# Kernel tuning notes

Measured on AMD Instinct MI355X. Metric: run time of the kernel, lower is better.

Reference implementation:

```python
import jax, jax.numpy as jnp
import numpy as np

NUM_HEADS = 16
ROPE_BASE = 10000.0

def rotate_half(x):
    h = x.shape[-1] // 2
    return jnp.concatenate([-x[..., h:], x[..., :h]], axis=-1)

def rope_cos_sin(seq_len, head_dim, dtype):
    inv_freq = 1.0 / (ROPE_BASE ** (jnp.arange(0, head_dim, 2, dtype=jnp.float32) / head_dim))
    t = jnp.arange(seq_len, dtype=jnp.float32)
    freqs = jnp.outer(t, inv_freq)              # [N, hd/2]
    emb = jnp.concatenate([freqs, freqs], -1)   # [N, hd]
    return jnp.cos(emb).astype(dtype), jnp.sin(emb).astype(dtype)

def setup_inputs() -> dict:
    key = jax.random.key(0)
    ks = jax.random.split(key, 5)
    B, N, D = 2, 2048, 1024
    s = 1.0 / np.sqrt(D)
    return {
        "x": jax.random.normal(ks[0], (B, N, D), jnp.float32),
        "attention_mask": jnp.ones((B, N), jnp.int32),
        "Wq": jax.random.normal(ks[1], (D, D), jnp.float32) * s,
        "Wk": jax.random.normal(ks[2], (D, D), jnp.float32) * s,
        "Wv": jax.random.normal(ks[3], (D, D), jnp.float32) * s,
        "Wo": jax.random.normal(ks[4], (D, D), jnp.float32) * s,
    }

def reference(x, attention_mask, Wq, Wk, Wv, Wo):
    B, N, D = x.shape
    H = NUM_HEADS
    hd = D // H
    scale = hd ** -0.5
    # projections (nn.Linear: x @ W.T), split heads -> [B, H, N, hd]
    q = jnp.einsum('bnd,ed->bne', x, Wq).reshape(B, N, H, hd).transpose(0, 2, 1, 3)
    k = jnp.einsum('bnd,ed->bne', x, Wk).reshape(B, N, H, hd).transpose(0, 2, 1, 3)
    v = jnp.einsum('bnd,ed->bne', x, Wv).reshape(B, N, H, hd).transpose(0, 2, 1, 3)
    cos, sin = rope_cos_sin(N, hd, x.dtype)     # [N, hd]
    cos = cos[None, None]; sin = sin[None, None]
    q = q * cos + rotate_half(q) * sin
    k = k * cos + rotate_half(k) * sin
    attn = jnp.einsum('bhqd,bhkd->bhqk', q, k) * scale
    mask = attention_mask.astype(bool)[:, None, None, :]        # [B,1,1,N]
    attn = jnp.where(mask, attn, -jnp.inf)
    all_masked = (attention_mask.sum(-1) == 0)[:, None, None, None]
    attn = jnp.where(all_masked, 0.0, attn)
    attn = jax.nn.softmax(attn, axis=-1)
    out = jnp.einsum('bhqk,bhkd->bhqd', attn, v)
    out = out.transpose(0, 2, 1, 3).reshape(B, N, D)
    return jnp.einsum('bnd,ed->bne', out, Wo)
```

## Files before the change

kernel.cpp:

```cpp
#include <hip/hip_runtime.h>
#include <math.h>

#define BATCH 2
#define SEQ   2048
#define DM    1024
#define NH    16
#define HD    64
#define MTOT  (BATCH*SEQ)

typedef short v8s __attribute__((ext_vector_type(8)));
typedef short v4s __attribute__((ext_vector_type(4)));
typedef float v4f __attribute__((ext_vector_type(4)));

#define MFMA16(a, b, c) __builtin_amdgcn_mfma_f32_16x16x32_bf16((a), (b), (c), 0, 0, 0)

__device__ __forceinline__ short f2b(float f) {
    union { float f; unsigned u; } v; v.f = f;
    return (short)((v.u + 0x8000u) >> 16);
}

__device__ __forceinline__ float fexp2(float x) {
    float r; asm("v_exp_f32 %0, %1" : "=v"(r) : "v"(x)); return r;
}

__device__ __forceinline__ void gload16(const void* g, void* lds) {
    __builtin_amdgcn_global_load_lds(
        (const __attribute__((address_space(1))) void*)g,
        (__attribute__((address_space(3))) void*)lds, 16, 0, 0);
}

__device__ __forceinline__ void rope_cs(int n, float f_rev, float* c, float* s) {
    float rev = (float)n * f_rev;
    float t = rev - floorf(rev);
    float ang = t * 6.283185307179586f;
    *c = __cosf(ang);
    *s = __sinf(ang);
}

#define L2_1E4_D32 0.4152410118609203f
#define INV2PI     0.15915494309189535f
#define QSCALE     0.18033688011112042f

__global__ __launch_bounds__(256) void cvt_all_kernel(
    const float* __restrict__ x,  const float* __restrict__ wq,
    const float* __restrict__ wk, const float* __restrict__ wv,
    const float* __restrict__ wo, short* __restrict__ dst)
{
    int i = blockIdx.x * 256 + threadIdx.x;
    const float* src; int off;
    if (i < (1 << 19)) { src = x; off = i; }
    else {
        int j = i - (1 << 19);
        int wsel = j >> 17;
        off = j & ((1 << 17) - 1);
        src = (wsel == 0) ? wq : (wsel == 1) ? wk : (wsel == 2) ? wv : wo;
    }
    const float4* s4 = (const float4*)src;
    float4 a = s4[2 * off], b = s4[2 * off + 1];
    v8s p;
    p[0] = f2b(a.x); p[1] = f2b(a.y); p[2] = f2b(a.z); p[3] = f2b(a.w);
    p[4] = f2b(b.x); p[5] = f2b(b.y); p[6] = f2b(b.z); p[7] = f2b(b.w);
    *(v8s*)&dst[8 * i] = p;
}

__global__ __launch_bounds__(256, 3) void qkv_rope_mfma(
    const short* __restrict__ xb, const short* __restrict__ Wqb,
    const short* __restrict__ Wkb, const short* __restrict__ Wvb,
    short* __restrict__ K, short* __restrict__ Vt, short* __restrict__ Qb)
{
    const int zz = blockIdx.z;
    const short* __restrict__ Wb = (zz == 0) ? Wkb : (zz == 1) ? Wvb : Wqb;
    const int m0 = blockIdx.x * 128, e00 = blockIdx.y * 128;
    const int tid = threadIdx.x;
    const int w = tid >> 6, lane = tid & 63, lq = lane >> 4, lr = lane & 15;
    const int wm = w >> 1, wn = w & 1;

    __shared__ union {
        struct { short As[128][32]; short Bs[128][32]; } p1;
        short Css[128][136];
    } u;

    v4f acc[4][4];
    #pragma unroll
    for (int i = 0; i < 4; ++i)
        for (int j = 0; j < 4; ++j)
            for (int r = 0; r < 4; ++r) acc[i][j][r] = 0.f;

    const int gr = lane >> 2, gc = 8 * (lane & 3);
    for (int k0 = 0; k0 < DM; k0 += 32) {
        __syncthreads();
        gload16(&xb[(size_t)(m0 + 32 * w      + gr) * DM + k0 + gc], &u.p1.As[32 * w][0]);
        gload16(&xb[(size_t)(m0 + 32 * w + 16 + gr) * DM + k0 + gc], &u.p1.As[32 * w + 16][0]);
        gload16(&Wb[(size_t)(e00 + 32 * w      + gr) * DM + k0 + gc], &u.p1.Bs[32 * w][0]);
        gload16(&Wb[(size_t)(e00 + 32 * w + 16 + gr) * DM + k0 + gc], &u.p1.Bs[32 * w + 16][0]);
        __syncthreads();
        v8s af[4], bf[4];
        #pragma unroll
        for (int i = 0; i < 4; ++i)
            af[i] = *(const v8s*)&u.p1.As[64 * wm + 16 * i + lr][8 * lq];
        #pragma unroll
        for (int j = 0; j < 4; ++j)
            bf[j] = *(const v8s*)&u.p1.Bs[64 * wn + 16 * j + lr][8 * lq];
        #pragma unroll
        for (int i = 0; i < 4; ++i)
            #pragma unroll
            for (int j = 0; j < 4; ++j)
                acc[i][j] = MFMA16(af[i], bf[j], acc[i][j]);
    }
    __syncthreads();

    const int b = m0 >> 11, n00 = m0 & (SEQ - 1);

    if (zz != 1) {
        short* __restrict__ dst = (zz == 0) ? K : Qb;
        const float sc = (zz == 0) ? 1.0f : QSCALE;
        float f0 = exp2f(-(float)lr * L2_1E4_D32) * INV2PI;
        float f1 = exp2f(-(float)(16 + lr) * L2_1E4_D32) * INV2PI;
        #pragma unroll
        for (int i = 0; i < 4; ++i) {
            #pragma unroll
            for (int r = 0; r < 4; ++r) {
                int row = 64 * wm + 16 * i + 4 * lq + r;
                int n = n00 + row;
                float c0v, s0v, c1v, s1v;
                rope_cs(n, f0, &c0v, &s0v);
                rope_cs(n, f1, &c1v, &s1v);
                float q0 = acc[i][0][r], q1 = acc[i][1][r];
                float q2 = acc[i][2][r], q3 = acc[i][3][r];
                u.Css[row][64 * wn + lr]      = f2b(sc * (q0 * c0v - q2 * s0v));
                u.Css[row][64 * wn + 16 + lr] = f2b(sc * (q1 * c1v - q3 * s1v));
                u.Css[row][64 * wn + 32 + lr] = f2b(sc * (q2 * c0v + q0 * s0v));
                u.Css[row][64 * wn + 48 + lr] = f2b(sc * (q3 * c1v + q1 * s1v));
            }
        }
        __syncthreads();
        int row = tid >> 1, hh = tid & 1;
        int h = (e00 >> 6) + hh;
        int n = n00 + row;
        size_t base = (((size_t)(b * NH + h)) * SEQ + n) * HD;
        #pragma unroll
        for (int p = 0; p < 8; ++p)
            *(v8s*)&dst[base + 8 * p] = *(const v8s*)&u.Css[row][64 * hh + 8 * p];
    } else {
        #pragma unroll
        for (int i = 0; i < 4; ++i) {
            #pragma unroll
            for (int j = 0; j < 4; ++j) {
                v4s t;
                #pragma unroll
                for (int r = 0; r < 4; ++r) t[r] = f2b(acc[i][j][r]);
                *(v4s*)&u.Css[64 * wn + 16 * j + lr][64 * wm + 16 * i + 4 * lq] = t;
            }
        }
        __syncthreads();
        int c = tid >> 1, half = (tid & 1) * 64;
        int h = (e00 + c) >> 6, d = (e00 + c) & 63;
        size_t base = (((size_t)(b * NH + h)) * HD + d) * SEQ + n00 + half;
        #pragma unroll
        for (int p = 0; p < 8; ++p)
            *(v8s*)&Vt[base + 8 * p] = *(const v8s*)&u.Css[c][half + 8 * p];
    }
}

#define SWZ(tile, row, bo) ((char*)&(tile)[row][0] + ((bo) ^ (((row) & 7) << 4)))

__global__ __launch_bounds__(512, 4) void attn_mfma(
    const short* __restrict__ Qb, const short* __restrict__ K,
    const short* __restrict__ Vt, const int* __restrict__ mask,
    short* __restrict__ O)
{
    const int m0 = blockIdx.x * 128, h = blockIdx.y;
    const int b = m0 >> 11, n0 = m0 & (SEQ - 1), bh = b * NH + h;
    const int tid = threadIdx.x;
    const int w = tid >> 6, lane = tid & 63, lq = lane >> 4, lr = lane & 15;

    __shared__ short Ks[128][64];
    __shared__ short Vs[64][128];
    __shared__ short Ps[128][64];
    __shared__ float mbias[128];

    const short* __restrict__ Qh = Qb + (size_t)bh * SEQ * HD;
    v8s aq[2];
    #pragma unroll
    for (int ks = 0; ks < 2; ++ks)
        aq[ks] = *(const v8s*)&Qh[(size_t)(n0 + 16 * w + lr) * HD + 32 * ks + 8 * lq];

    float lacc[4] = {0.f, 0.f, 0.f, 0.f};
    v4f o[4];
    #pragma unroll
    for (int nt = 0; nt < 4; ++nt)
        for (int r = 0; r < 4; ++r) o[nt][r] = 0.f;

    const int kr = tid >> 2, kc = (tid & 3) * 16;
    const int kb = 32 * (tid & 3);
    const int krh = kr & 63;
    const int pkr = 64 * (kr >> 6) + 16 * (krh & 3) + (krh >> 2);
    const int vr = tid >> 3, vc = (tid & 7) * 16;
    const int vb = 32 * (tid & 7);
    const short* __restrict__ Kb = K + (size_t)bh * SEQ * HD;
    const short* __restrict__ Vb = Vt + (size_t)bh * HD * SEQ;

    v8s k1 = *(const v8s*)&Kb[(size_t)kr * HD + kc];
    v8s k2 = *(const v8s*)&Kb[(size_t)kr * HD + kc + 8];
    v8s v1 = *(const v8s*)&Vb[(size_t)vr * SEQ + vc];
    v8s v2 = *(const v8s*)&Vb[(size_t)vr * SEQ + vc + 8];
    int mnext = ((tid & 3) == 0) ? mask[b * SEQ + kr] : 0;

    for (int c0 = 0; c0 < SEQ; c0 += 128) {
        __syncthreads();
        *(v8s*)SWZ(Ks, pkr, kb)      = k1;
        *(v8s*)SWZ(Ks, pkr, kb + 16) = k2;
        *(v8s*)SWZ(Vs, vr, vb)       = v1;
        *(v8s*)SWZ(Vs, vr, vb + 16)  = v2;
        if ((tid & 3) == 0) mbias[pkr] = mnext ? -24.0f : -1e30f;
        __syncthreads();
        if (c0 + 128 < SEQ) {
            k1 = *(const v8s*)&Kb[(size_t)(c0 + 128 + kr) * HD + kc];
            k2 = *(const v8s*)&Kb[(size_t)(c0 + 128 + kr) * HD + kc + 8];
            v1 = *(const v8s*)&Vb[(size_t)vr * SEQ + c0 + 128 + vc];
            v2 = *(const v8s*)&Vb[(size_t)vr * SEQ + c0 + 128 + vc + 8];
            if ((tid & 3) == 0) mnext = mask[b * SEQ + c0 + 128 + kr];
        }

        #pragma unroll
        for (int half = 0; half < 2; ++half) {
            v8s kf[2][4];
            #pragma unroll
            for (int ks = 0; ks < 2; ++ks)
                #pragma unroll
                for (int nt = 0; nt < 4; ++nt)
                    kf[ks][nt] = *(const v8s*)SWZ(Ks, 64 * half + 16 * nt + lr,
                                                  64 * ks + 16 * lq);
            float bias[4];
            #pragma unroll
            for (int nt = 0; nt < 4; ++nt)
                bias[nt] = mbias[64 * half + 16 * nt + lr];

            v4f sv[4];
            #pragma unroll
            for (int nt = 0; nt < 4; ++nt)
                for (int r = 0; r < 4; ++r) sv[nt][r] = 0.f;
            #pragma unroll
            for (int ks = 0; ks < 2; ++ks)
                #pragma unroll
                for (int nt = 0; nt < 4; ++nt)
                    sv[nt] = MFMA16(aq[ks], kf[ks][nt], sv[nt]);

            #pragma unroll
            for (int r = 0; r < 4; ++r) {
                float p0 = fexp2(sv[0][r] + bias[0]);
                float p1 = fexp2(sv[1][r] + bias[1]);
                float p2 = fexp2(sv[2][r] + bias[2]);
                float p3 = fexp2(sv[3][r] + bias[3]);
                lacc[r] += (p0 + p1) + (p2 + p3);
                unsigned u0, u1;
                asm("v_cvt_pk_bf16_f32 %0, %1, %2" : "=v"(u0) : "v"(p0), "v"(p1));
                asm("v_cvt_pk_bf16_f32 %0, %1, %2" : "=v"(u1) : "v"(p2), "v"(p3));
                uint2 pk; pk.x = u0; pk.y = u1;
                int prow = 16 * w + 4 * lq + r;
                *(uint2*)SWZ(Ps, prow, 8 * lr) = pk;
            }
            #pragma unroll
            for (int ks = 0; ks < 2; ++ks) {
                v8s a = *(const v8s*)SWZ(Ps, 16 * w + lr, 64 * ks + 16 * lq);
                #pragma unroll
                for (int nt = 0; nt < 4; ++nt) {
                    v8s vf = *(const v8s*)SWZ(Vs, 16 * nt + lr,
                                              128 * half + 64 * ks + 16 * lq);
                    o[nt] = MFMA16(a, vf, o[nt]);
                }
            }
        }
    }

    #pragma unroll
    for (int r = 0; r < 4; ++r) {
        float l = lacc[r];
        l += __shfl_xor(l, 1);
        l += __shfl_xor(l, 2);
        l += __shfl_xor(l, 4);
        l += __shfl_xor(l, 8);
        float inv = (l > 0.f) ? 1.f / l : 0.f;
        int qrow = 16 * w + 4 * lq + r;
        #pragma unroll
        for (int nt = 0; nt < 4; ++nt)
            O[(size_t)(m0 + qrow) * DM + h * HD + 16 * nt + lr] =
                f2b(o[nt][r] * inv);
    }
}

__global__ __launch_bounds__(256, 2) void oproj_mfma(
    const short* __restrict__ O, const short* __restrict__ Wob,
    float* __restrict__ out)
{
    const int m0 = blockIdx.x * 64, e00 = blockIdx.y * 128;
    const int tid = threadIdx.x;
    const int w = tid >> 6, lane = tid & 63, lq = lane >> 4, lr = lane & 15;

    __shared__ short As[64][32];
    __shared__ short Bs[128][32];

    v4f acc[4][2];
    #pragma unroll
    for (int i = 0; i < 4; ++i)
        for (int j = 0; j < 2; ++j)
            for (int r = 0; r < 4; ++r) acc[i][j][r] = 0.f;

    const int gr = lane >> 2, gc = 8 * (lane & 3);
    for (int k0 = 0; k0 < DM; k0 += 32) {
        __syncthreads();
        gload16(&O[(size_t)(m0 + 16 * w + gr) * DM + k0 + gc],         &As[16 * w][0]);
        gload16(&Wob[(size_t)(e00 + 32 * w      + gr) * DM + k0 + gc], &Bs[32 * w][0]);
        gload16(&Wob[(size_t)(e00 + 32 * w + 16 + gr) * DM + k0 + gc], &Bs[32 * w + 16][0]);
        __syncthreads();
        v8s af[4], bf[2];
        #pragma unroll
        for (int i = 0; i < 4; ++i)
            af[i] = *(const v8s*)&As[16 * i + lr][8 * lq];
        #pragma unroll
        for (int j = 0; j < 2; ++j)
            bf[j] = *(const v8s*)&Bs[32 * w + 16 * j + lr][8 * lq];
        #pragma unroll
        for (int i = 0; i < 4; ++i)
            #pragma unroll
            for (int j = 0; j < 2; ++j)
                acc[i][j] = MFMA16(af[i], bf[j], acc[i][j]);
    }

    #pragma unroll
    for (int i = 0; i < 4; ++i)
        #pragma unroll
        for (int r = 0; r < 4; ++r) {
            int m = m0 + 16 * i + 4 * lq + r;
            #pragma unroll
            for (int j = 0; j < 2; ++j)
                out[(size_t)m * DM + e00 + 32 * w + 16 * j + lr] = acc[i][j][r];
        }
}

extern "C" void kernel_launch(void* const* d_in, const int* in_sizes, int n_in,
                              void* d_out, int out_size, void* d_ws, size_t ws_size,
                              hipStream_t stream)
{
    const float* x    = (const float*)d_in[0];
    const int*   mask = (const int*)d_in[1];
    const float* Wq   = (const float*)d_in[2];
    const float* Wk   = (const float*)d_in[3];
    const float* Wv   = (const float*)d_in[4];
    const float* Wo   = (const float*)d_in[5];
    float* out = (float*)d_out;

    short* xb  = (short*)d_ws;
    short* Wqb = xb  + (size_t)MTOT * DM;
    short* Wkb = Wqb + (size_t)DM * DM;
    short* Wvb = Wkb + (size_t)DM * DM;
    short* Wob = Wvb + (size_t)DM * DM;
    short* Qb  = Wob + (size_t)DM * DM;
    short* O   = xb;
    short* K  = (short*)d_out;
    short* Vt = K + (size_t)MTOT * DM;

    cvt_all_kernel<<<4096, 256, 0, stream>>>(x, Wq, Wk, Wv, Wo, xb);

    dim3 g1(MTOT / 128, DM / 128, 3);
    qkv_rope_mfma<<<g1, 256, 0, stream>>>(xb, Wqb, Wkb, Wvb, K, Vt, Qb);

    dim3 g2(MTOT / 128, NH);
    attn_mfma<<<g2, 512, 0, stream>>>(Qb, K, Vt, mask, O);

    dim3 g3(MTOT / 64, DM / 128);
    oproj_mfma<<<g3, 256, 0, stream>>>(O, Wob, out);
}
```

Baseline: 191.9 us.

## Split keys across wave pairs in attention with shared-memory reduction of partial outputs

Each wave now handles 32 query rows over half of each 128-key chunk, instead of 16 rows over the whole chunk. This lets each K and V fragment read from LDS feed two MFMAs, roughly halving LDS fragment traffic per MFMA, and it removes the inner half loop. The price is a doubled P tile in shared memory (larger LDS footprint, which may lower occupancy) and a final cross-wave reduction of partial outputs and row sums through shared memory, with extra barriers.

```diff
diff --git a/kernel.cpp b/kernel.cpp
--- a/kernel.cpp
+++ b/kernel.cpp
@@ -173,23 +173,31 @@
     const int b = m0 >> 11, n0 = m0 & (SEQ - 1), bh = b * NH + h;
     const int tid = threadIdx.x;
     const int w = tid >> 6, lane = tid & 63, lq = lane >> 4, lr = lane & 15;
+    const int wr = w >> 1, wk = w & 1;
 
     __shared__ short Ks[128][64];
     __shared__ short Vs[64][128];
-    __shared__ short Ps[128][64];
+    __shared__ short Ps[128][128];
     __shared__ float mbias[128];
 
     const short* __restrict__ Qh = Qb + (size_t)bh * SEQ * HD;
-    v8s aq[2];
-    #pragma unroll
-    for (int ks = 0; ks < 2; ++ks)
-        aq[ks] = *(const v8s*)&Qh[(size_t)(n0 + 16 * w + lr) * HD + 32 * ks + 8 * lq];
-
-    float lacc[4] = {0.f, 0.f, 0.f, 0.f};
-    v4f o[4];
-    #pragma unroll
-    for (int nt = 0; nt < 4; ++nt)
-        for (int r = 0; r < 4; ++r) o[nt][r] = 0.f;
+    v8s aq[2][2];
+    #pragma unroll
+    for (int it = 0; it < 2; ++it)
+        #pragma unroll
+        for (int ks = 0; ks < 2; ++ks)
+            aq[it][ks] = *(const v8s*)&Qh[(size_t)(n0 + 32 * wr + 16 * it + lr) * HD
+                                          + 32 * ks + 8 * lq];
+
+    float lacc[2][4];
+    v4f o[2][4];
+    #pragma unroll
+    for (int it = 0; it < 2; ++it)
+        #pragma unroll
+        for (int nt = 0; nt < 4; ++nt) {
+            lacc[it][nt] = 0.f;
+            for (int r = 0; r < 4; ++r) o[it][nt][r] = 0.f;
+        }
 
     const int kr = tid >> 2, kc = (tid & 3) * 16;
     const int kb = 32 * (tid & 3);
@@ -223,69 +231,103 @@
         }
 
         #pragma unroll
-        for (int half = 0; half < 2; ++half) {
-            v8s kf[2][4];
-            #pragma unroll
-            for (int ks = 0; ks < 2; ++ks)
+        for (int ntp = 0; ntp < 2; ++ntp) {
+            v8s kf0[2], kf1[2];
+            #pragma unroll
+            for (int ks = 0; ks < 2; ++ks) {
+                kf0[ks] = *(const v8s*)SWZ(Ks, 64 * wk + 32 * ntp + lr,
+                                           64 * ks + 16 * lq);
+                kf1[ks] = *(const v8s*)SWZ(Ks, 64 * wk + 32 * ntp + 16 + lr,
+                                           64 * ks + 16 * lq);
+            }
+            float bias0 = mbias[64 * wk + 32 * ntp + lr];
+            float bias1 = mbias[64 * wk + 32 * ntp + 16 + lr];
+            #pragma unroll
+            for (int it = 0; it < 2; ++it) {
+                v4f s0, s1;
+                #pragma unroll
+                for (int r = 0; r < 4; ++r) { s0[r] = 0.f; s1[r] = 0.f; }
+                #pragma unroll
+                for (int ks = 0; ks < 2; ++ks) {
+                    s0 = MFMA16(aq[it][ks], kf0[ks], s0);
+                    s1 = MFMA16(aq[it][ks], kf1[ks], s1);
+                }
+                #pragma unroll
+                for (int r = 0; r < 4; ++r) {
+                    float p0 = fexp2(s0[r] + bias0);
+                    float p1 = fexp2(s1[r] + bias1);
+                    lacc[it][r] += p0 + p1;
+                    unsigned uu;
+                    asm("v_cvt_pk_bf16_f32 %0, %1, %2" : "=v"(uu) : "v"(p0), "v"(p1));
+                    int qrow = 32 * wr + 16 * it + 4 * lq + r;
+                    *(unsigned*)SWZ(Ps, qrow, 128 * wk + 8 * lr + 4 * ntp) = uu;
+                }
+            }
+        }
+
+        #pragma unroll
+        for (int ks = 0; ks < 2; ++ks) {
+            v8s a0 = *(const v8s*)SWZ(Ps, 32 * wr + lr,
+                                      128 * wk + 64 * ks + 16 * lq);
+            v8s a1 = *(const v8s*)SWZ(Ps, 32 * wr + 16 + lr,
+                                      128 * wk + 64 * ks + 16 * lq);
+            #pragma unroll
+            for (int nt = 0; nt < 4; ++nt) {
+                v8s vf = *(const v8s*)SWZ(Vs, 16 * nt + lr,
+                                          128 * wk + 64 * ks + 16 * lq);
+                o[0][nt] = MFMA16(a0, vf, o[0][nt]);
+                o[1][nt] = MFMA16(a1, vf, o[1][nt]);
+            }
+        }
+    }
+
+    #pragma unroll
+    for (int it = 0; it < 2; ++it)
+        #pragma unroll
+        for (int r = 0; r < 4; ++r) {
+            float l = lacc[it][r];
+            l += __shfl_xor(l, 1);
+            l += __shfl_xor(l, 2);
+            l += __shfl_xor(l, 4);
+            l += __shfl_xor(l, 8);
+            lacc[it][r] = l;
+        }
+
+    __syncthreads();
+    float* mO = (float*)&Ps[0][0];
+    float* mL = (float*)&Ks[0][0];
+    if (wk == 1) {
+        #pragma unroll
+        for (int it = 0; it < 2; ++it) {
+            #pragma unroll
+            for (int nt = 0; nt < 4; ++nt)
+                *(v4f*)&mO[(((wr * 8 + it * 4 + nt) * 64) + lane) * 4] = o[it][nt];
+            #pragma unroll
+            for (int r = 0; r < 4; ++r)
+                mL[(wr * 8 + it * 4 + r) * 64 + lane] = lacc[it][r];
+        }
+    }
+    __syncthreads();
+    if (wk == 0) {
+        #pragma unroll
+        for (int it = 0; it < 2; ++it) {
+            #pragma unroll
+            for (int nt = 0; nt < 4; ++nt) {
+                v4f t = *(const v4f*)&mO[(((wr * 8 + it * 4 + nt) * 64) + lane) * 4];
+                #pragma unroll
+                for (int r = 0; r < 4; ++r) o[it][nt][r] += t[r];
+            }
+            #pragma unroll
+            for (int r = 0; r < 4; ++r) {
+                float l = lacc[it][r] + mL[(wr * 8 + it * 4 + r) * 64 + lane];
+                float inv = (l > 0.f) ? 1.f / l : 0.f;
+                int qrow = 32 * wr + 16 * it + 4 * lq + r;
                 #pragma unroll
                 for (int nt = 0; nt < 4; ++nt)
-                    kf[ks][nt] = *(const v8s*)SWZ(Ks, 64 * half + 16 * nt + lr,
-                                                  64 * ks + 16 * lq);
-            float bias[4];
-            #pragma unroll
-            for (int nt = 0; nt < 4; ++nt)
-                bias[nt] = mbias[64 * half + 16 * nt + lr];
-
-            v4f sv[4];
-            #pragma unroll
-            for (int nt = 0; nt < 4; ++nt)
-                for (int r = 0; r < 4; ++r) sv[nt][r] = 0.f;
-            #pragma unroll
-            for (int ks = 0; ks < 2; ++ks)
-                #pragma unroll
-                for (int nt = 0; nt < 4; ++nt)
-                    sv[nt] = MFMA16(aq[ks], kf[ks][nt], sv[nt]);
-
-            #pragma unroll
-            for (int r = 0; r < 4; ++r) {
-                float p0 = fexp2(sv[0][r] + bias[0]);
-                float p1 = fexp2(sv[1][r] + bias[1]);
-                float p2 = fexp2(sv[2][r] + bias[2]);
-                float p3 = fexp2(sv[3][r] + bias[3]);
-                lacc[r] += (p0 + p1) + (p2 + p3);
-                unsigned u0, u1;
-                asm("v_cvt_pk_bf16_f32 %0, %1, %2" : "=v"(u0) : "v"(p0), "v"(p1));
-                asm("v_cvt_pk_bf16_f32 %0, %1, %2" : "=v"(u1) : "v"(p2), "v"(p3));
-                uint2 pk; pk.x = u0; pk.y = u1;
-                int prow = 16 * w + 4 * lq + r;
-                *(uint2*)SWZ(Ps, prow, 8 * lr) = pk;
-            }
-            #pragma unroll
-            for (int ks = 0; ks < 2; ++ks) {
-                v8s a = *(const v8s*)SWZ(Ps, 16 * w + lr, 64 * ks + 16 * lq);
-                #pragma unroll
-                for (int nt = 0; nt < 4; ++nt) {
-                    v8s vf = *(const v8s*)SWZ(Vs, 16 * nt + lr,
-                                              128 * half + 64 * ks + 16 * lq);
-                    o[nt] = MFMA16(a, vf, o[nt]);
-                }
-            }
-        }
-    }
-
-    #pragma unroll
-    for (int r = 0; r < 4; ++r) {
-        float l = lacc[r];
-        l += __shfl_xor(l, 1);
-        l += __shfl_xor(l, 2);
-        l += __shfl_xor(l, 4);
-        l += __shfl_xor(l, 8);
-        float inv = (l > 0.f) ? 1.f / l : 0.f;
-        int qrow = 16 * w + 4 * lq + r;
-        #pragma unroll
-        for (int nt = 0; nt < 4; ++nt)
-            O[(size_t)(m0 + qrow) * DM + h * HD + 16 * nt + lr] =
-                f2b(o[nt][r] * inv);
+                    O[(size_t)(m0 + qrow) * DM + h * HD + 16 * nt + lr] =
+                        f2b(o[it][nt][r] * inv);
+            }
+        }
     }
 }
 
```

New measurement: 243.6 us. 26.9% more time.
